# Performance work log

Hardware: AMD Instinct MI355X
Metric: run time of the kernel (lower is better)

Reference implementation:

```python
import math
import jax, jax.numpy as jnp
import numpy as np

B, T, C = 2, 2048, 1024
H, N1, N2, N3 = 16, 6, 4, 6
HD = C // H  # 64


def setup_inputs() -> dict:
    key = jax.random.key(0)
    k1, k2, k3 = jax.random.split(key, 3)
    return {
        "x": jax.random.normal(k1, (B, T, C), jnp.float32),
        "qkv_w": jax.random.normal(k2, (3 * C, C), jnp.float32) * (C ** -0.5),
        "proj_w": jax.random.normal(k3, (C, C), jnp.float32) * (C ** -0.5),
        "proj_b": jnp.zeros((C,), jnp.float32),
        "curvature": jnp.ones((1, N2, 1, 1), jnp.float32),
    }


def _rotary(T_, hd, dtype):
    inv_freq = 1.0 / (10000.0 ** (jnp.arange(0, hd, 2, dtype=jnp.float32) / hd))
    freqs = jnp.outer(jnp.arange(T_, dtype=jnp.float32), inv_freq)  # [T, hd/2]
    return jnp.cos(freqs)[None, :, None, :].astype(dtype), jnp.sin(freqs)[None, :, None, :].astype(dtype)


def _apply_rot(x, cos, sin):
    x1, x2 = x[..., : x.shape[-1] // 2], x[..., x.shape[-1] // 2 :]
    return jnp.concatenate([x1 * cos + x2 * sin, -x1 * sin + x2 * cos], axis=-1).astype(x.dtype)


def _causal_bias(L, S, dtype):
    mask = jnp.triu(jnp.ones((L, S), bool), k=1)
    return jnp.where(mask, jnp.asarray(-jnp.inf, dtype), jnp.asarray(0.0, dtype))


def _sdpa(q, k, v, scale):
    # q,k,v: [B,h,T,hd]
    scores = jnp.einsum("bhtd,bhsd->bhts", q, k) * scale + _causal_bias(q.shape[-2], k.shape[-2], q.dtype)
    return jnp.einsum("bhts,bhsd->bhtd", jax.nn.softmax(scores, axis=-1), v)


def _hyp_attn(q, k, v, curv):
    # Lorentz-model hyperbolic attention. project(x,k) = [sqrt(1/k+||x||^2), x];
    # d(u,v) = sqrt(1/k) * arccosh(-k * <u,v>_L), <u,v>_L = -u0 v0 + <u_s, v_s>.
    eps = 1e-6
    tq = jnp.sqrt(1.0 / curv + jnp.sum(q * q, axis=-1, keepdims=True))  # [B,h,T,1]
    tk = jnp.sqrt(1.0 / curv + jnp.sum(k * k, axis=-1, keepdims=True))  # [B,h,S,1]
    inner = jnp.einsum("bhtd,bhsd->bhts", q, k) - tq * jnp.swapaxes(tk, -1, -2)  # Lorentz inner [B,h,T,S]
    arg = jnp.maximum(-curv * inner, 1.0 + 1e-7)
    dis = jnp.sqrt(1.0 / curv) * jnp.arccosh(arg)
    scores = 1.0 / (eps + dis) + _causal_bias(q.shape[-2], k.shape[-2], q.dtype)
    return jnp.einsum("bhts,bhsd->bhtd", jax.nn.softmax(scores, axis=-1), v)


def reference(x, qkv_w, proj_w, proj_b, curvature):
    Bx, Tx, Cx = x.shape
    qkv = x @ qkv_w.T  # [B,T,3C]
    q, k, v = jnp.split(qkv, 3, axis=-1)
    q = q.reshape(Bx, Tx, H, HD)
    k = k.reshape(Bx, Tx, H, HD)
    v = v.reshape(Bx, Tx, H, HD)
    cos, sin = _rotary(Tx, HD, x.dtype)
    q = _apply_rot(q, cos, sin)
    k = _apply_rot(k, cos, sin)
    # -> [B,H,T,hd]
    q, k, v = (jnp.swapaxes(t, 1, 2) for t in (q, k, v))
    outs = []
    # euclidean heads
    outs.append(_sdpa(q[:, :N1], k[:, :N1], v[:, :N1], 1.0 / math.sqrt(HD)))
    # hyperbolic heads
    outs.append(_hyp_attn(q[:, N1 : N1 + N2], k[:, N1 : N1 + N2], v[:, N1 : N1 + N2], curvature))
    # spherical heads (cosine-sim attention, scale = sqrt(head_dim))
    qn = q[:, N1 + N2 :] / jnp.maximum(jnp.linalg.norm(q[:, N1 + N2 :], axis=-1, keepdims=True), 1e-12)
    kn = k[:, N1 + N2 :] / jnp.maximum(jnp.linalg.norm(k[:, N1 + N2 :], axis=-1, keepdims=True), 1e-12)
    outs.append(_sdpa(qn, kn, v[:, N1 + N2 :], math.sqrt(HD)))
    y = jnp.concatenate(outs, axis=1)  # [B,H,T,hd]
    y = jnp.swapaxes(y, 1, 2).reshape(Bx, Tx, Cx)
    return y @ proj_w.T + proj_b
```

## Files before the change

kernel.cpp:

```cpp
#include <hip/hip_runtime.h>
#include <stdint.h>
#include <math.h>


typedef __bf16 bf16x8 __attribute__((ext_vector_type(8)));
typedef float f32x4 __attribute__((ext_vector_type(4)));

static __device__ __forceinline__ float bf2f(unsigned short u) {
  union { unsigned int i; float f; } v; v.i = ((unsigned int)u) << 16; return v.f;
}
static __device__ __forceinline__ unsigned short f2bf(float f) {
  union { float f; unsigned int i; } v; v.f = f;
  unsigned int x = v.i;
  x += 0x7fffu + ((x >> 16) & 1u);
  return (unsigned short)(x >> 16);
}

static __device__ __forceinline__ void async_copy16(const void* gsrc, void* ldst) {
  auto* lp = reinterpret_cast<__attribute__((address_space(3))) unsigned int*>(
      reinterpret_cast<uintptr_t>(ldst));
  auto* gp = reinterpret_cast<const __attribute__((address_space(1))) unsigned int*>(
      reinterpret_cast<uintptr_t>(gsrc));
  __builtin_amdgcn_global_load_lds(gp, lp, 16, 0, 0);
}

template <int PAT>
__global__ __launch_bounds__(256) void split2(const float* __restrict__ in,
                                              unsigned short* __restrict__ out) {
  const int row = blockIdx.x;
  const int kq = threadIdx.x * 4;
  const f32x4 x = *(const f32x4*)(in + (size_t)row * 1024 + kq);
  unsigned short hi[4], lo[4];
#pragma unroll
  for (int i = 0; i < 4; ++i) {
    hi[i] = f2bf(x[i]);
    lo[i] = f2bf(x[i] - bf2f(hi[i]));
  }
  uint2 uh, ul;
  uh.x = (unsigned)hi[0] | ((unsigned)hi[1] << 16);
  uh.y = (unsigned)hi[2] | ((unsigned)hi[3] << 16);
  ul.x = (unsigned)lo[0] | ((unsigned)lo[1] << 16);
  ul.y = (unsigned)lo[2] | ((unsigned)lo[3] << 16);
  unsigned short* op = out + (size_t)row * 2048 + kq;
  *(uint2*)(op)        = uh;
  *(uint2*)(op + 1024) = PAT ? uh : ul;
}

template <int HASBIAS>
__global__ __launch_bounds__(256) void gemm_bt(
    const unsigned short* __restrict__ A, const unsigned short* __restrict__ Bm,
    float* __restrict__ C, const float* __restrict__ bias, int N_, int K_) {
  alignas(16) __shared__ unsigned short smA[128 * 64];
  alignas(16) __shared__ unsigned short smB[128 * 64];
  const int tid = threadIdx.x;
  const int lane = tid & 63;
  const int wv = tid >> 6;
  const int wm = wv >> 1, wn = wv & 1;
  const long m0 = (long)blockIdx.y * 128, n0 = (long)blockIdx.x * 128;

  const f32x4 zero4 = {0.f, 0.f, 0.f, 0.f};
  f32x4 acc[4][4];
#pragma unroll
  for (int i = 0; i < 4; ++i)
#pragma unroll
    for (int j = 0; j < 4; ++j) acc[i][j] = zero4;

  int mrow[4], gg[4];
#pragma unroll
  for (int w = 0; w < 4; ++w) {
    int c = w * 256 + tid;
    mrow[w] = c >> 3;
    gg[w] = (c & 7) ^ ((c >> 3) & 7);
  }

  const int kTiles = K_ >> 6;
  for (int kt = 0; kt < kTiles; ++kt) {
    if (kt) __syncthreads();
    const int kb = kt << 6;
#pragma unroll
    for (int w = 0; w < 4; ++w) {
      const int c = w * 256 + tid;
      async_copy16(A + (size_t)(m0 + mrow[w]) * K_ + kb + gg[w] * 8,
                   (char*)smA + c * 16);
      async_copy16(Bm + (size_t)(n0 + mrow[w]) * K_ + kb + gg[w] * 8,
                   (char*)smB + c * 16);
    }
    __syncthreads();
#pragma unroll
    for (int ks = 0; ks < 2; ++ks) {
      bf16x8 af[4], bg[4];
#pragma unroll
      for (int i = 0; i < 4; ++i) {
        const int ra = wm * 64 + i * 16 + (lane & 15);
        const int ga = (ks * 4 + (lane >> 4)) ^ (ra & 7);
        af[i] = *(const bf16x8*)((const char*)smA + ra * 128 + ga * 16);
        const int rb = wn * 64 + i * 16 + (lane & 15);
        const int gb2 = (ks * 4 + (lane >> 4)) ^ (rb & 7);
        bg[i] = *(const bf16x8*)((const char*)smB + rb * 128 + gb2 * 16);
      }
#pragma unroll
      for (int i = 0; i < 4; ++i)
#pragma unroll
        for (int j = 0; j < 4; ++j)
          acc[i][j] = __builtin_amdgcn_mfma_f32_16x16x32_bf16(af[i], bg[j], acc[i][j], 0, 0, 0);
    }
  }

  const int r0 = wm * 64 + (lane >> 4) * 4;
  const int c0 = wn * 64 + (lane & 15);
#pragma unroll
  for (int j = 0; j < 4; ++j) {
    const long col = n0 + c0 + j * 16;
    float bv = 0.f;
    if (HASBIAS) bv = bias[col];
#pragma unroll
    for (int i = 0; i < 4; ++i) {
#pragma unroll
      for (int r = 0; r < 4; ++r) {
        const long row = m0 + r0 + i * 16 + r;
        C[row * N_ + col] = acc[i][j][r] + bv;
      }
    }
  }
}

__global__ __launch_bounds__(256) void prep(
    const float* __restrict__ qkvf, unsigned short* __restrict__ Q2,
    unsigned short* __restrict__ K2, unsigned short* __restrict__ V2,
    float* __restrict__ qq, float* __restrict__ kk, const float* __restrict__ curvg) {
  __shared__ unsigned short Vl[64 * 66];
  const int tid = threadIdx.x;
  const int zz = blockIdx.x;
  const int ttile = zz & 31, bh = zz >> 5;
  const int b = bh >> 4, h = bh & 15;
  const int t0 = ttile * 64;
  const int tr = tid >> 2, seg = tid & 3;
  const int t = t0 + tr;
  const float* src = qkvf + ((size_t)(b * 2048 + t)) * 3072 + h * 64 + seg * 16;

  float qv[16], kv[16], vv[16];
#pragma unroll
  for (int c = 0; c < 4; ++c) {
    const f32x4 a  = *(const f32x4*)(src + c * 4);
    const f32x4 bb = *(const f32x4*)(src + 1024 + c * 4);
    const f32x4 cc = *(const f32x4*)(src + 2048 + c * 4);
#pragma unroll
    for (int e = 0; e < 4; ++e) { qv[c*4+e] = a[e]; kv[c*4+e] = bb[e]; vv[c*4+e] = cc[e]; }
  }
  float qr[16], kr[16];
#pragma unroll
  for (int e = 0; e < 16; ++e) {
    const int d = seg * 16 + e;
    const int i = d & 31;
    const float invf = exp2f(-0.41524101186109286f * (float)i);
    float sn, cs;
    sincosf((float)t * invf, &sn, &cs);
    const float qo = __shfl_xor(qv[e], 2, 64);
    const float ko = __shfl_xor(kv[e], 2, 64);
    qr[e] = (d < 32) ? (qv[e] * cs + qo * sn) : (qv[e] * cs - qo * sn);
    kr[e] = (d < 32) ? (kv[e] * cs + ko * sn) : (kv[e] * cs - ko * sn);
  }
  float sq = 0.f, sk = 0.f;
#pragma unroll
  for (int e = 0; e < 16; ++e) { sq += qr[e] * qr[e]; sk += kr[e] * kr[e]; }
  sq += __shfl_xor(sq, 1, 64); sq += __shfl_xor(sq, 2, 64);
  sk += __shfl_xor(sk, 1, 64); sk += __shfl_xor(sk, 2, 64);
  float qscale = 0.125f * 1.4426950408889634f;
  if (h >= 10) {
    const float rq = 1.0f / fmaxf(sqrtf(sq), 1e-12f);
    const float rk = 1.0f / fmaxf(sqrtf(sk), 1e-12f);
#pragma unroll
    for (int e = 0; e < 16; ++e) { qr[e] *= rq; kr[e] *= rk; }
    qscale = 8.0f * 1.4426950408889634f;
  } else if (h >= 6) {
    qscale = 1.0f;
  }
#pragma unroll
  for (int e = 0; e < 16; ++e) qr[e] *= qscale;
  if (seg == 0) {
    const int idx = b * 32768 + h * 2048 + t;
    float oq = sq, ok = sk;
    if (h >= 6 && h < 10) {
      const float invc = 1.0f / curvg[h - 6];
      oq = sqrtf(invc + sq);
      ok = sqrtf(invc + sk);
    }
    qq[idx] = oq;
    kk[idx] = ok;
  }
  const int st = seg >> 1;
  const int quadA = (seg * 2) & 3, quadB = (seg * 2 + 1) & 3;
  {
    unsigned int wh[8], wl[8];
#pragma unroll
    for (int p = 0; p < 8; ++p) {
      unsigned short h0 = f2bf(qr[2*p]), h1 = f2bf(qr[2*p+1]);
      unsigned short l0 = f2bf(qr[2*p] - bf2f(h0)), l1 = f2bf(qr[2*p+1] - bf2f(h1));
      wh[p] = (unsigned)h0 | ((unsigned)h1 << 16);
      wl[p] = (unsigned)l0 | ((unsigned)l1 << 16);
    }
    const int qi = (t >> 4) & 1, c15q = t & 15;
    unsigned short* qs = Q2 + ((size_t)bh * 64 + (t >> 5)) * 4096;
    const int fh = ((qi * 2 + st) * 2 + 0) * 512, fl = fh + 512;
    *(uint4*)(qs + fh + quadA * 128 + c15q * 8) = uint4{wh[0], wh[1], wh[2], wh[3]};
    *(uint4*)(qs + fh + quadB * 128 + c15q * 8) = uint4{wh[4], wh[5], wh[6], wh[7]};
    *(uint4*)(qs + fl + quadA * 128 + c15q * 8) = uint4{wl[0], wl[1], wl[2], wl[3]};
    *(uint4*)(qs + fl + quadB * 128 + c15q * 8) = uint4{wl[4], wl[5], wl[6], wl[7]};
#pragma unroll
    for (int p = 0; p < 8; ++p) {
      unsigned short h0 = f2bf(kr[2*p]), h1 = f2bf(kr[2*p+1]);
      wh[p] = (unsigned)h0 | ((unsigned)h1 << 16);
    }
    const int kj = (tr >> 4) & 3, c15k = tr & 15;
    unsigned short* ks = K2 + ((size_t)bh * 32 + ttile) * 4096;
    const int gh = (st * 4 + kj) * 512;
    *(uint4*)(ks + gh + quadA * 128 + c15k * 8) = uint4{wh[0], wh[1], wh[2], wh[3]};
    *(uint4*)(ks + gh + quadB * 128 + c15k * 8) = uint4{wh[4], wh[5], wh[6], wh[7]};
  }
#pragma unroll
  for (int e = 0; e < 16; ++e) Vl[(seg * 16 + e) * 66 + tr] = f2bf(vv[e]);
  __syncthreads();
  {
    const int d = tid >> 2, tch = (tid & 3) * 16;
    unsigned int wv2[8];
#pragma unroll
    for (int p = 0; p < 8; ++p) {
      const unsigned short a0 = Vl[d * 66 + tch + 2*p];
      const unsigned short a1 = Vl[d * 66 + tch + 2*p + 1];
      wv2[p] = (unsigned)a0 | ((unsigned)a1 << 16);
    }
    const int dj = d >> 4, c15v = d & 15;
    const int ks2 = tch >> 5;
    const int qvA = (tch >> 3) & 3, qvB = ((tch >> 3) + 1) & 3;
    unsigned short* vs = V2 + ((size_t)bh * 32 + ttile) * 4096 + (ks2 * 4 + dj) * 512;
    *(uint4*)(vs + qvA * 128 + c15v * 8) = uint4{wv2[0], wv2[1], wv2[2], wv2[3]};
    *(uint4*)(vs + qvB * 128 + c15v * 8) = uint4{wv2[4], wv2[5], wv2[6], wv2[7]};
  }
}

__global__ __launch_bounds__(256, 2) void attn_part(
    const unsigned short* __restrict__ Q2, const unsigned short* __restrict__ K2,
    const unsigned short* __restrict__ V2, const float* __restrict__ tqq,
    const float* __restrict__ tkk, const float* __restrict__ curvg,
    float* __restrict__ part) {
  const int tid = threadIdx.x;
  const int lane = tid & 63;
  const int wv = tid >> 6;
  const int quad = lane >> 4, c15 = lane & 15;
  const int z = blockIdx.x * 4 + wv;
  const int bh = z / 160;
  const int u = 159 - (z - bh * 160);
  int qw, ch;
  if (u < 16)      { qw = u; ch = 0; }
  else if (u < 48) { qw = 16 + ((u - 16) >> 1); ch = (u - 16) & 1; }
  else if (u < 96) { const int s2 = u - 48; const int q3 = s2 / 3; qw = 32 + q3; ch = s2 - 3 * q3; }
  else             { const int s2 = u - 96; qw = 48 + (s2 >> 2); ch = s2 & 3; }
  const int h = bh & 15;
  const int geom = (h < 6) ? 0 : ((h < 10) ? 1 : 2);
  const int qrow0 = qw * 32;
  const f32x4 zero4 = {0.f, 0.f, 0.f, 0.f};

  const unsigned short* qbase = Q2 + ((size_t)bh * 64 + qw) * 4096;
  bf16x8 qh[2][2], ql[2][2];
#pragma unroll
  for (int qi = 0; qi < 2; ++qi)
#pragma unroll
    for (int st = 0; st < 2; ++st) {
      const int f = ((qi * 2 + st) * 2) * 512 + lane * 8;
      qh[qi][st] = *(const bf16x8*)(qbase + f);
      ql[qi][st] = *(const bf16x8*)(qbase + f + 512);
    }

  float curv = 1.f, sic = 1.f;
  const float Moff = 4.0f;
  float tqs[2] = {0.f, 0.f};
  if (geom == 1) {
    curv = curvg[h - 6];
    sic = sqrtf(1.0f / curv);
#pragma unroll
    for (int qi = 0; qi < 2; ++qi)
      tqs[qi] = tqq[bh * 2048 + qrow0 + qi * 16 + c15];
  }

  const __bf16 one_b = (__bf16)1.0f;
  const bf16x8 ones = {one_b, one_b, one_b, one_b, one_b, one_b, one_b, one_b};

  const int iA = ((quad & 1) * 32 + c15) * 4;
  const int iB = iA + 64;
  const bool hiq = (quad >= 2);

  f32x4 o[2][4];
  f32x4 ol[2] = {zero4, zero4};
#pragma unroll
  for (int qi = 0; qi < 2; ++qi)
#pragma unroll
    for (int dj = 0; dj < 4; ++dj) o[qi][dj] = zero4;

  const int nkt = (qw >> 1) + 1;
  const int ktB = ch * 8;
  const int ktE = (ktB + 8 < nkt) ? (ktB + 8) : nkt;
  for (int kt = ktB; kt < ktE; ++kt) {
    const int kb = kt * 64;
    const unsigned short* kbase = K2 + ((size_t)bh * 32 + kt) * 4096;
    const unsigned short* vbase = V2 + ((size_t)bh * 32 + kt) * 4096;

    bf16x8 kf[2][4], vf[2][4];
#pragma unroll
    for (int st = 0; st < 2; ++st)
#pragma unroll
      for (int kj = 0; kj < 4; ++kj)
        kf[st][kj] = *(const bf16x8*)(kbase + (st * 4 + kj) * 512 + lane * 8);
#pragma unroll
    for (int ks2 = 0; ks2 < 2; ++ks2)
#pragma unroll
      for (int dj = 0; dj < 4; ++dj)
        vf[ks2][dj] = *(const bf16x8*)(vbase + (ks2 * 4 + dj) * 512 + lane * 8);
    f32x4 tk4[4];
    if (geom == 1) {
#pragma unroll
      for (int kj = 0; kj < 4; ++kj)
        tk4[kj] = *(const f32x4*)(tkk + bh * 2048 + kb + kj * 16 + quad * 4);
    }

    f32x4 s[2][4];
#pragma unroll
    for (int qi = 0; qi < 2; ++qi)
#pragma unroll
      for (int kj = 0; kj < 4; ++kj) s[qi][kj] = zero4;
    __builtin_amdgcn_s_setprio(1);
#pragma unroll
    for (int st = 0; st < 2; ++st) {
#pragma unroll
      for (int kj = 0; kj < 4; ++kj) {
#pragma unroll
        for (int qi = 0; qi < 2; ++qi) {
          s[qi][kj] = __builtin_amdgcn_mfma_f32_16x16x32_bf16(kf[st][kj], qh[qi][st], s[qi][kj], 0, 0, 0);
          s[qi][kj] = __builtin_amdgcn_mfma_f32_16x16x32_bf16(kf[st][kj], ql[qi][st], s[qi][kj], 0, 0, 0);
        }
      }
    }
    __builtin_amdgcn_s_setprio(0);

    const bool needmask = (kt == nkt - 1);
    unsigned pw[2][4][2];
#pragma unroll
    for (int qi = 0; qi < 2; ++qi) {
      const int qcol = qrow0 + qi * 16 + c15;
#pragma unroll
      for (int kj = 0; kj < 4; ++kj) {
        const int kloc = kb + kj * 16 + quad * 4;
        const f32x4 d4 = s[qi][kj];
        f32x4 p;
        if (geom == 1) {
          const float tq = tqs[qi];
#pragma unroll
          for (int r = 0; r < 4; ++r) {
            const float a = fmaxf(curv * (tq * tk4[kj][r] - d4[r]), 1.0f + 1e-7f);
            const float dis = sic * __logf(a + sqrtf(a * a - 1.0f));
            p[r] = __expf(__builtin_amdgcn_rcpf(1e-6f + dis) - Moff);
          }
        } else {
#pragma unroll
          for (int r = 0; r < 4; ++r) p[r] = exp2f(d4[r]);
        }
        if (needmask) {
#pragma unroll
          for (int r = 0; r < 4; ++r)
            if (kloc + r > qcol) p[r] = 0.0f;
        }
        union { float f; unsigned u2; } b0, b1, b2, b3;
        b0.f = p[0]; b1.f = p[1]; b2.f = p[2]; b3.f = p[3];
        pw[qi][kj][0] = (b0.u2 >> 16) | (b1.u2 & 0xffff0000u);
        pw[qi][kj][1] = (b2.u2 >> 16) | (b3.u2 & 0xffff0000u);
      }
    }

    __builtin_amdgcn_s_setprio(1);
#pragma unroll
    for (int ks2 = 0; ks2 < 2; ++ks2) {
      const int a = ks2 * 2, b2 = ks2 * 2 + 1;
#pragma unroll
      for (int qi = 0; qi < 2; ++qi) {
        const int w0A = __builtin_amdgcn_ds_bpermute(iA, (int)pw[qi][a][0]);
        const int w0B = __builtin_amdgcn_ds_bpermute(iA, (int)pw[qi][b2][0]);
        const int w1A = __builtin_amdgcn_ds_bpermute(iA, (int)pw[qi][a][1]);
        const int w1B = __builtin_amdgcn_ds_bpermute(iA, (int)pw[qi][b2][1]);
        const int w2A = __builtin_amdgcn_ds_bpermute(iB, (int)pw[qi][a][0]);
        const int w2B = __builtin_amdgcn_ds_bpermute(iB, (int)pw[qi][b2][0]);
        const int w3A = __builtin_amdgcn_ds_bpermute(iB, (int)pw[qi][a][1]);
        const int w3B = __builtin_amdgcn_ds_bpermute(iB, (int)pw[qi][b2][1]);
        union { uint4 u; bf16x8 v; } pf;
        pf.u.x = (unsigned)(hiq ? w0B : w0A);
        pf.u.y = (unsigned)(hiq ? w1B : w1A);
        pf.u.z = (unsigned)(hiq ? w2B : w2A);
        pf.u.w = (unsigned)(hiq ? w3B : w3A);
        const bf16x8 pfrag = pf.v;
        ol[qi] = __builtin_amdgcn_mfma_f32_16x16x32_bf16(ones, pfrag, ol[qi], 0, 0, 0);
#pragma unroll
        for (int dj = 0; dj < 4; ++dj)
          o[qi][dj] = __builtin_amdgcn_mfma_f32_16x16x32_bf16(vf[ks2][dj], pfrag, o[qi][dj], 0, 0, 0);
      }
    }
    __builtin_amdgcn_s_setprio(0);
  }

  float* slot = part + (size_t)(bh * 160 + u) * 2112;
#pragma unroll
  for (int qi = 0; qi < 2; ++qi)
#pragma unroll
    for (int dj = 0; dj < 4; ++dj)
      *(f32x4*)(slot + (qi * 4 + dj) * 256 + lane * 4) = o[qi][dj];
  if (quad == 0) {
#pragma unroll
    for (int qi = 0; qi < 2; ++qi)
      slot[2048 + qi * 16 + c15] = ol[qi][0];
  }
}

__global__ __launch_bounds__(256) void attn_reduce(
    const float* __restrict__ part, unsigned short* __restrict__ Ay) {
  __shared__ float Ol[4][32 * 65];
  const int tid = threadIdx.x;
  const int lane = tid & 63;
  const int wv = tid >> 6;
  float* Olw = &Ol[wv][0];
  const int quad = lane >> 4, c15 = lane & 15;
  const int z = blockIdx.x * 4 + wv, bh = z & 31, qw = 63 - (z >> 5);
  const int b = bh >> 4, h = bh & 15;
  const int G = qw >> 4;
  const int base = qw + 8 * G * (G - 1) + (qw & 15) * G;
  const float* slot0 = part + (size_t)(bh * 160 + base) * 2112;

  const f32x4 zero4 = {0.f, 0.f, 0.f, 0.f};
  f32x4 o[8];
  float ls[2] = {0.f, 0.f};
#pragma unroll
  for (int i = 0; i < 8; ++i) o[i] = zero4;
  for (int chv = 0; chv <= G; ++chv) {
    const float* sl = slot0 + chv * 2112;
#pragma unroll
    for (int i = 0; i < 8; ++i) o[i] += *(const f32x4*)(sl + i * 256 + lane * 4);
#pragma unroll
    for (int qi = 0; qi < 2; ++qi)
      ls[qi] += sl[2048 + qi * 16 + c15];
  }
#pragma unroll
  for (int qi = 0; qi < 2; ++qi) {
    const float invl = __builtin_amdgcn_rcpf(ls[qi]);
#pragma unroll
    for (int dj = 0; dj < 4; ++dj) {
      const f32x4 val = o[qi * 4 + dj] * invl;
#pragma unroll
      for (int r = 0; r < 4; ++r)
        Olw[(qi * 16 + c15) * 65 + dj * 16 + quad * 4 + r] = val[r];
    }
  }
  __syncthreads();
  const int row = lane >> 1, half = lane & 1;
  const float* rp = Olw + row * 65 + half * 32;
  unsigned int uh[16], ul2[16];
#pragma unroll
  for (int p = 0; p < 16; ++p) {
    const float v0 = rp[2 * p], v1 = rp[2 * p + 1];
    const unsigned short h0 = f2bf(v0), h1 = f2bf(v1);
    const unsigned short g0 = f2bf(v0 - bf2f(h0)), g1 = f2bf(v1 - bf2f(h1));
    uh[p] = (unsigned)h0 | ((unsigned)h1 << 16);
    ul2[p] = (unsigned)g0 | ((unsigned)g1 << 16);
  }
  unsigned short* yp = Ay + ((size_t)(b * 2048 + qw * 32 + row)) * 2048 + h * 64 + half * 32;
#pragma unroll
  for (int c = 0; c < 4; ++c) {
    *(uint4*)(yp + 8 * c)        = uint4{uh[4*c], uh[4*c+1], uh[4*c+2], uh[4*c+3]};
    *(uint4*)(yp + 1024 + 8 * c) = uint4{ul2[4*c], ul2[4*c+1], ul2[4*c+2], ul2[4*c+3]};
  }
}

extern "C" void kernel_launch(void* const* d_in, const int* in_sizes, int n_in,
                              void* d_out, int out_size, void* d_ws, size_t ws_size,
                              hipStream_t stream) {
  const float* x      = (const float*)d_in[0];
  const float* qkv_w  = (const float*)d_in[1];
  const float* proj_w = (const float*)d_in[2];
  const float* proj_b = (const float*)d_in[3];
  const float* curvature = (const float*)d_in[4];
  float* out = (float*)d_out;

  char* ws = (char*)d_ws;
  unsigned short* AX   = (unsigned short*)ws;
  unsigned short* BW   = (unsigned short*)(ws + 16777216);
  float*          QKVF = (float*)(ws + 33554432);
  unsigned short* Q2   = (unsigned short*)ws;
  unsigned short* K2   = (unsigned short*)(ws + 16777216);
  unsigned short* V2   = (unsigned short*)(ws + 25165824);
  float*          PART = (float*)(ws + 33554432);
  unsigned short* BPW  = (unsigned short*)(ws + 76808192);
  unsigned short* AY   = (unsigned short*)ws;
  float*          QQ   = (float*)(ws + 94371840);
  float*          KK   = (float*)(ws + 94633984);

  split2<0><<<4096, 256, 0, stream>>>(x, AX);
  split2<1><<<3072, 256, 0, stream>>>(qkv_w, BW);

  gemm_bt<0><<<dim3(24, 32), 256, 0, stream>>>(AX, BW, QKVF, nullptr, 3072, 2048);

  prep<<<1024, 256, 0, stream>>>(QKVF, Q2, K2, V2, QQ, KK, curvature);

  split2<1><<<1024, 256, 0, stream>>>(proj_w, BPW);

  attn_part<<<1280, 256, 0, stream>>>(Q2, K2, V2, QQ, KK, curvature, PART);

  attn_reduce<<<512, 256, 0, stream>>>(PART, AY);

  gemm_bt<1><<<dim3(8, 32), 256, 0, stream>>>(AY, BPW, out, proj_b, 1024, 2048);
}
```

Before: 285.2 us.

## Share single bf16 weight tile across hi/lo activation halves in split GEMM

The GEMMs emulated fp32 with a K-concatenated layout: activations split as [hi, lo] and weights duplicated as [hi, hi], which doubled the weight load and the K loop length. Weights are now converted to one bf16 copy, and the kernel loads the hi and lo activation tiles into separate shared buffers so each weight fragment is reused for two MFMAs. This halves weight conversion, traffic and LDS loads for B while keeping the MFMA count the same. A blockIdx remap that groups workgroups into eight strided sets is also added, apparently to place neighbouring tiles on the same XCD for better L2 reuse.

```diff
diff --git a/kernel.cpp b/kernel.cpp
--- a/kernel.cpp
+++ b/kernel.cpp
@@ -46,17 +46,33 @@
   *(uint2*)(op + 1024) = PAT ? uh : ul;
 }
 
+__global__ __launch_bounds__(256) void split1(const float* __restrict__ in,
+                                              unsigned short* __restrict__ out) {
+  const int row = blockIdx.x;
+  const int kq = threadIdx.x * 4;
+  const f32x4 x = *(const f32x4*)(in + (size_t)row * 1024 + kq);
+  uint2 uh;
+  uh.x = (unsigned)f2bf(x[0]) | ((unsigned)f2bf(x[1]) << 16);
+  uh.y = (unsigned)f2bf(x[2]) | ((unsigned)f2bf(x[3]) << 16);
+  *(uint2*)(out + (size_t)row * 1024 + kq) = uh;
+}
+
 template <int HASBIAS>
-__global__ __launch_bounds__(256) void gemm_bt(
+__global__ __launch_bounds__(256) void gemm_bt2(
     const unsigned short* __restrict__ A, const unsigned short* __restrict__ Bm,
-    float* __restrict__ C, const float* __restrict__ bias, int N_, int K_) {
-  alignas(16) __shared__ unsigned short smA[128 * 64];
-  alignas(16) __shared__ unsigned short smB[128 * 64];
+    float* __restrict__ C, const float* __restrict__ bias,
+    int NX, int N_, int Kr) {
+  alignas(16) __shared__ unsigned short smAh[128 * 64];
+  alignas(16) __shared__ unsigned short smAl[128 * 64];
+  alignas(16) __shared__ unsigned short smB [128 * 64];
   const int tid = threadIdx.x;
   const int lane = tid & 63;
-  const int wv = tid >> 6;
-  const int wm = wv >> 1, wn = wv & 1;
-  const long m0 = (long)blockIdx.y * 128, n0 = (long)blockIdx.x * 128;
+  const int wvi = tid >> 6;
+  const int wm = wvi >> 1, wn = wvi & 1;
+  const int cpx = gridDim.x >> 3;
+  const int wgid = ((int)blockIdx.x & 7) * cpx + ((int)blockIdx.x >> 3);
+  const long m0 = (long)(wgid / NX) * 128, n0 = (long)(wgid % NX) * 128;
+  const int K2w = Kr * 2;
 
   const f32x4 zero4 = {0.f, 0.f, 0.f, 0.f};
   f32x4 acc[4][4];
@@ -73,27 +89,29 @@
     gg[w] = (c & 7) ^ ((c >> 3) & 7);
   }
 
-  const int kTiles = K_ >> 6;
+  const int kTiles = Kr >> 6;
   for (int kt = 0; kt < kTiles; ++kt) {
     if (kt) __syncthreads();
     const int kb = kt << 6;
 #pragma unroll
     for (int w = 0; w < 4; ++w) {
       const int c = w * 256 + tid;
-      async_copy16(A + (size_t)(m0 + mrow[w]) * K_ + kb + gg[w] * 8,
-                   (char*)smA + c * 16);
-      async_copy16(Bm + (size_t)(n0 + mrow[w]) * K_ + kb + gg[w] * 8,
+      const size_t arow = (size_t)(m0 + mrow[w]) * K2w + kb + gg[w] * 8;
+      async_copy16(A + arow,        (char*)smAh + c * 16);
+      async_copy16(A + arow + Kr,   (char*)smAl + c * 16);
+      async_copy16(Bm + (size_t)(n0 + mrow[w]) * Kr + kb + gg[w] * 8,
                    (char*)smB + c * 16);
     }
     __syncthreads();
 #pragma unroll
     for (int ks = 0; ks < 2; ++ks) {
-      bf16x8 af[4], bg[4];
+      bf16x8 afh[4], afl[4], bg[4];
 #pragma unroll
       for (int i = 0; i < 4; ++i) {
         const int ra = wm * 64 + i * 16 + (lane & 15);
         const int ga = (ks * 4 + (lane >> 4)) ^ (ra & 7);
-        af[i] = *(const bf16x8*)((const char*)smA + ra * 128 + ga * 16);
+        afh[i] = *(const bf16x8*)((const char*)smAh + ra * 128 + ga * 16);
+        afl[i] = *(const bf16x8*)((const char*)smAl + ra * 128 + ga * 16);
         const int rb = wn * 64 + i * 16 + (lane & 15);
         const int gb2 = (ks * 4 + (lane >> 4)) ^ (rb & 7);
         bg[i] = *(const bf16x8*)((const char*)smB + rb * 128 + gb2 * 16);
@@ -101,8 +119,10 @@
 #pragma unroll
       for (int i = 0; i < 4; ++i)
 #pragma unroll
-        for (int j = 0; j < 4; ++j)
-          acc[i][j] = __builtin_amdgcn_mfma_f32_16x16x32_bf16(af[i], bg[j], acc[i][j], 0, 0, 0);
+        for (int j = 0; j < 4; ++j) {
+          acc[i][j] = __builtin_amdgcn_mfma_f32_16x16x32_bf16(afh[i], bg[j], acc[i][j], 0, 0, 0);
+          acc[i][j] = __builtin_amdgcn_mfma_f32_16x16x32_bf16(afl[i], bg[j], acc[i][j], 0, 0, 0);
+        }
     }
   }
 
@@ -487,29 +507,29 @@
 
   char* ws = (char*)d_ws;
   unsigned short* AX   = (unsigned short*)ws;
-  unsigned short* BW   = (unsigned short*)(ws + 16777216);
+  unsigned short* BW1  = (unsigned short*)(ws + 16777216);
   float*          QKVF = (float*)(ws + 33554432);
   unsigned short* Q2   = (unsigned short*)ws;
   unsigned short* K2   = (unsigned short*)(ws + 16777216);
   unsigned short* V2   = (unsigned short*)(ws + 25165824);
   float*          PART = (float*)(ws + 33554432);
-  unsigned short* BPW  = (unsigned short*)(ws + 76808192);
+  unsigned short* BPW1 = (unsigned short*)(ws + 76808192);
   unsigned short* AY   = (unsigned short*)ws;
   float*          QQ   = (float*)(ws + 94371840);
   float*          KK   = (float*)(ws + 94633984);
 
   split2<0><<<4096, 256, 0, stream>>>(x, AX);
-  split2<1><<<3072, 256, 0, stream>>>(qkv_w, BW);
-
-  gemm_bt<0><<<dim3(24, 32), 256, 0, stream>>>(AX, BW, QKVF, nullptr, 3072, 2048);
+  split1<<<3072, 256, 0, stream>>>(qkv_w, BW1);
+
+  gemm_bt2<0><<<768, 256, 0, stream>>>(AX, BW1, QKVF, nullptr, 24, 3072, 1024);
 
   prep<<<1024, 256, 0, stream>>>(QKVF, Q2, K2, V2, QQ, KK, curvature);
 
-  split2<1><<<1024, 256, 0, stream>>>(proj_w, BPW);
+  split1<<<1024, 256, 0, stream>>>(proj_w, BPW1);
 
   attn_part<<<1280, 256, 0, stream>>>(Q2, K2, V2, QQ, KK, curvature, PART);
 
   attn_reduce<<<512, 256, 0, stream>>>(PART, AY);
 
-  gemm_bt<1><<<dim3(8, 32), 256, 0, stream>>>(AY, BPW, out, proj_b, 1024, 2048);
-}
+  gemm_bt2<1><<<256, 256, 0, stream>>>(AY, BPW1, out, proj_b, 8, 1024, 1024);
+}
```

Result: faster. 278.3 us (-2.4%).
